# Performance work log

Measured on AMD Instinct MI355X. Metric: run time of the kernel, lower is better.

## Reference

```python
import jax, jax.numpy as jnp
import numpy as np

B, P, E, H = 16, 1024, 1024, 16
DH = E // H  # 64


def setup_inputs() -> dict:
    key = jax.random.key(0)
    ks = jax.random.split(key, 7)
    # kaiming_uniform on [H, DH, DH]: bound = sqrt(6 / fan_in), fan_in = DH
    bound = float(np.sqrt(6.0 / DH))
    w_att_val = jax.random.uniform(ks[0], (H, DH, DH), jnp.float32, -bound, bound)
    attention_bias = jax.random.normal(ks[1], (H, P, P), jnp.float32)
    lb = float(1.0 / np.sqrt(E))
    wv_w = jax.random.uniform(ks[2], (E, E), jnp.float32, -lb, lb)
    wv_b = jax.random.uniform(ks[3], (E,), jnp.float32, -lb, lb)
    out_w = jax.random.uniform(ks[4], (E, E), jnp.float32, -lb, lb)
    out_b = jax.random.uniform(ks[5], (E,), jnp.float32, -lb, lb)
    x = jax.random.normal(ks[6], (B, P, E), jnp.float32)
    return {"x": x, "w_att_val": w_att_val, "attention_bias": attention_bias,
            "wv_w": wv_w, "wv_b": wv_b, "out_w": out_w, "out_b": out_b}


def reference(x, w_att_val, attention_bias, wv_w, wv_b, out_w, out_b):
    b, p, e = x.shape
    dh = e // H
    # split heads: [B, H, P, DH]
    x_h = x.reshape(b, p, H, dh).transpose(0, 2, 1, 3)
    # bilinear scores: (x_h @ W) @ x_h^T -> [B, H, P, P]
    xw = jnp.einsum('bhpd,hde->bhpe', x_h, w_att_val)
    scores = jnp.einsum('bhpe,bhqe->bhpq', xw, x_h)
    scores = scores / jnp.sqrt(jnp.asarray(dh, x.dtype)) + attention_bias
    attn = jax.nn.softmax(scores, axis=-1)
    # values: Linear(E, E) then split heads
    vx = x @ wv_w.T + wv_b
    vx = vx.reshape(b, p, H, dh).transpose(0, 2, 1, 3)
    out = jnp.einsum('bhpq,bhqd->bhpd', attn, vx)
    out = out.transpose(0, 2, 1, 3).reshape(b, p, e)
    return out @ out_w.T + out_b
```

## Files before the change

kernel.cpp:

```cpp
#include <hip/hip_runtime.h>

#define PB 16
#define PP 1024
#define PE 1024
#define PH 16
#define PDH 64

typedef __attribute__((ext_vector_type(8))) short bf16x8;
typedef __attribute__((ext_vector_type(4))) short bf16x4;
typedef __attribute__((ext_vector_type(4))) float f32x4;

#define LOG2E 1.44269504088896340736f

__device__ __forceinline__ short f2bf(float f) {
    union { float f; unsigned u; } a;
    a.f = f;
    unsigned u = a.u;
    u += 0x7fffu + ((u >> 16) & 1u);
    return (short)(u >> 16);
}
__device__ __forceinline__ float bf2f(short s) {
    union { unsigned u; float f; } a;
    a.u = ((unsigned)(unsigned short)s) << 16;
    return a.f;
}
__device__ __forceinline__ unsigned cvtpk(float lo, float hi) {
    unsigned r;
    asm("v_cvt_pk_bf16_f32 %0, %1, %2" : "=v"(r) : "v"(lo), "v"(hi));
    return r;
}
union U8 { unsigned u[4]; bf16x8 v; };
__device__ __forceinline__ void async16(const void* g, void* l) {
    __builtin_amdgcn_global_load_lds(
        (const __attribute__((address_space(1))) unsigned int*)g,
        (__attribute__((address_space(3))) unsigned int*)l, 16, 0, 0);
}

__global__ __launch_bounds__(256) void bias_prep(const float* __restrict__ bias,
                                                 short* __restrict__ biasP) {
    int bid = blockIdx.x;
    int h = bid >> 7, qblk = (bid >> 4) & 7, tile = bid & 15;
    int q0 = qblk * 128, kv0 = tile * 64;
    __shared__ short T[128][68];

    int t = threadIdx.x;
    {
        int qr = t >> 1, half = t & 1;
        const float* src = bias + ((size_t)h << 20) + (size_t)(q0 + qr) * 1024 + kv0 + half * 32;
#pragma unroll
        for (int i = 0; i < 32; i += 4) {
            float4 v = *(const float4*)(src + i);
            bf16x4 p = {f2bf(v.x * LOG2E), f2bf(v.y * LOG2E), f2bf(v.z * LOG2E), f2bf(v.w * LOG2E)};
            *(bf16x4*)&T[qr][half * 32 + i] = p;
        }
    }
    __syncthreads();

    int w = t >> 6, l = t & 63, lm = l & 15, lq = l >> 4;
    short* dst = biasP + (((size_t)(h * 16 + tile) * 8 + qblk) * 4 + w) * 2048 + l * 8;
#pragma unroll
    for (int j = 0; j < 4; j++) {
        bf16x4 a = *(const bf16x4*)&T[w * 32 + lm][j * 16 + lq * 4];
        bf16x4 b = *(const bf16x4*)&T[w * 32 + 16 + lm][j * 16 + lq * 4];
        bf16x8 o = {a[0], a[1], a[2], a[3], b[0], b[1], b[2], b[3]};
        *(bf16x8*)(dst + j * 512) = o;
    }
}

__global__ __launch_bounds__(256) void wconv(const float* __restrict__ wvw,
                                             const float* __restrict__ outw,
                                             short* __restrict__ wvwb,
                                             short* __restrict__ outwb) {
    int bid = blockIdx.x;
    const float* src = (bid < 512) ? wvw : outw;
    short* dst = (bid < 512) ? wvwb : outwb;
    int lb = (bid < 512) ? bid : bid - 512;
    size_t idx = ((size_t)lb * 256 + threadIdx.x) * 8;
    float4 a = *(const float4*)(src + idx);
    float4 b = *(const float4*)(src + idx + 4);
    bf16x8 t = {f2bf(a.x), f2bf(a.y), f2bf(a.z), f2bf(a.w),
                f2bf(b.x), f2bf(b.y), f2bf(b.z), f2bf(b.w)};
    *(bf16x8*)(dst + idx) = t;
}

__global__ __launch_bounds__(256) void xw_kernel(const float* __restrict__ x,
                                                 const float* __restrict__ watt,
                                                 short* __restrict__ xw,
                                                 short* __restrict__ xbf) {
    int bid = blockIdx.x;
    int q4 = bid & 3;
    int bh = bid >> 2;
    int h = bh & 15;
    __shared__ short Wt[64][88];

    int tid = threadIdx.x;
    {
        const float* W = watt + (size_t)h * 4096;
        int idx = tid * 16;
        int d = idx >> 6, e0 = idx & 63;
#pragma unroll
        for (int i = 0; i < 16; i += 4) {
            float4 v = *(const float4*)(W + d * 64 + e0 + i);
            Wt[e0 + i + 0][d] = f2bf(v.x);
            Wt[e0 + i + 1][d] = f2bf(v.y);
            Wt[e0 + i + 2][d] = f2bf(v.z);
            Wt[e0 + i + 3][d] = f2bf(v.w);
        }
    }
    __syncthreads();

    int wave = tid >> 6, lane = tid & 63;
    int lm = lane & 15, lq = lane >> 4;

    bf16x8 bfr[4][2];
#pragma unroll
    for (int nt = 0; nt < 4; nt++)
#pragma unroll
        for (int kf = 0; kf < 2; kf++)
            bfr[nt][kf] = *(const bf16x8*)&Wt[nt * 16 + lm][kf * 32 + lq * 8];

    int b = bh >> 4;
    const float QSCALE = 0.125f * LOG2E;
    for (int pass = 0; pass < 4; pass++) {
        int p0 = q4 * 256 + pass * 64 + wave * 16;
        const float* xrow = x + ((size_t)(b * 1024 + p0 + lm)) * 1024 + h * 64;
        short* xorow = xbf + ((size_t)(b * 1024 + p0 + lm)) * 1024 + h * 64;
        bf16x8 af[2];
#pragma unroll
        for (int kf = 0; kf < 2; kf++) {
            float4 v0 = *(const float4*)(xrow + kf * 32 + lq * 8);
            float4 v1 = *(const float4*)(xrow + kf * 32 + lq * 8 + 4);
            bf16x8 t;
            t[0] = f2bf(v0.x); t[1] = f2bf(v0.y); t[2] = f2bf(v0.z); t[3] = f2bf(v0.w);
            t[4] = f2bf(v1.x); t[5] = f2bf(v1.y); t[6] = f2bf(v1.z); t[7] = f2bf(v1.w);
            af[kf] = t;
            *(bf16x8*)(xorow + kf * 32 + lq * 8) = t;
        }
#pragma unroll
        for (int nt = 0; nt < 4; nt++) {
            f32x4 acc = {0.f, 0.f, 0.f, 0.f};
            acc = __builtin_amdgcn_mfma_f32_16x16x32_bf16(af[0], bfr[nt][0], acc, 0, 0, 0);
            acc = __builtin_amdgcn_mfma_f32_16x16x32_bf16(af[1], bfr[nt][1], acc, 0, 0, 0);
            size_t base = ((size_t)bh * 1024 + p0 + lq * 4) * 64 + nt * 16 + lm;
#pragma unroll
            for (int r = 0; r < 4; r++)
                xw[base + (size_t)r * 64] = f2bf(acc[r] * QSCALE);
        }
    }
}

__global__ __launch_bounds__(256) void vx_gemm(const short* __restrict__ xbf,
                                               const short* __restrict__ wvwb,
                                               const float* __restrict__ wvb,
                                               short* __restrict__ vt) {
    int logical = (blockIdx.x & 7) * 128 + (blockIdx.x >> 3);
    int mblk = logical >> 3, nblk = logical & 7;
    int m0 = mblk * 128, n0 = nblk * 128;
    __shared__ short As[128 * 32];
    __shared__ short Bs[128 * 32];

    int tid = threadIdx.x;
    int wv = tid >> 6, ln = tid & 63;
    int c0 = wv * 2;
    int rrow = ln >> 2, rseg = (ln & 3) * 8;
    const short* gA = xbf + (size_t)(m0 + c0 * 16 + rrow) * 1024 + rseg;
    const short* gB = wvwb + (size_t)(n0 + c0 * 16 + rrow) * 1024 + rseg;
    short* lA = As + c0 * 512;
    short* lB = Bs + c0 * 512;

    int lane = ln, lm = lane & 15, lq = lane >> 4;
    int wm = (wv >> 1) * 64, wn = (wv & 1) * 64;

    f32x4 acc[4][4];
#pragma unroll
    for (int i = 0; i < 4; i++)
#pragma unroll
        for (int j = 0; j < 4; j++) acc[i][j] = (f32x4){0.f, 0.f, 0.f, 0.f};

    for (int k0 = 0; k0 < 1024; k0 += 32) {
        __syncthreads();
        async16(gA + k0, lA);
        async16(gA + k0 + 16 * 1024, lA + 512);
        async16(gB + k0, lB);
        async16(gB + k0 + 16 * 1024, lB + 512);
        __syncthreads();
        bf16x8 af[4], bfr[4];
#pragma unroll
        for (int mt = 0; mt < 4; mt++) af[mt] = *(const bf16x8*)&As[(wm + mt * 16 + lm) * 32 + lq * 8];
#pragma unroll
        for (int nt = 0; nt < 4; nt++) bfr[nt] = *(const bf16x8*)&Bs[(wn + nt * 16 + lm) * 32 + lq * 8];
#pragma unroll
        for (int mt = 0; mt < 4; mt++)
#pragma unroll
            for (int nt = 0; nt < 4; nt++)
                acc[mt][nt] = __builtin_amdgcn_mfma_f32_16x16x32_bf16(af[mt], bfr[nt], acc[mt][nt], 0, 0, 0);
    }

#pragma unroll
    for (int nt = 0; nt < 4; nt++) {
        int e = n0 + wn + nt * 16 + lm;
        float bias = wvb[e];
        int hh = e >> 6, dd = e & 63;
#pragma unroll
        for (int mt = 0; mt < 4; mt++) {
            int pg = m0 + wm + mt * 16 + lq * 4;
            int bb = pg >> 10, pp = pg & 1023;
            bf16x4 pk;
#pragma unroll
            for (int r = 0; r < 4; r++) pk[r] = f2bf(acc[mt][nt][r] + bias);
            *(bf16x4*)(vt + ((size_t)((bb * 16 + hh) * 64 + dd)) * 1024 + pp) = pk;
        }
    }
}

__global__ __launch_bounds__(256, 3) void flash_kernel(const short* __restrict__ xbf,
                                                       const short* __restrict__ xw,
                                                       const short* __restrict__ vt,
                                                       const short* __restrict__ biasP,
                                                       short* __restrict__ obuf) {
    int logical = (blockIdx.x & 7) * 256 + (blockIdx.x >> 3);
    int qblk = logical & 7, b = (logical >> 3) & 15, h = logical >> 7;
    int bh = b * 16 + h;
    int q0 = qblk * 128;

    __shared__ short Ks[64][72];
    __shared__ short Vs[64][72];
    __shared__ float Rs[4][36];

    int tid = threadIdx.x, wave = tid >> 6, lane = tid & 63;
    int lm = lane & 15, lq = lane >> 4;

    bf16x8 qa[2][2];
#pragma unroll
    for (int qt = 0; qt < 2; qt++)
#pragma unroll
        for (int kf = 0; kf < 2; kf++)
            qa[qt][kf] = *(const bf16x8*)(xw + ((size_t)bh * 1024 + q0 + wave * 32 + qt * 16 + lm) * 64 + kf * 32 + lq * 8);

    f32x4 o[2][4];
#pragma unroll
    for (int qt = 0; qt < 2; qt++)
#pragma unroll
        for (int dt = 0; dt < 4; dt++) o[qt][dt] = (f32x4){0.f, 0.f, 0.f, 0.f};
    float rs[2] = {0.f, 0.f};

    int ci0 = tid * 2, ci1 = tid * 2 + 1;
    int r0 = ci0 >> 3, s0 = (ci0 & 7) * 8;
    int r1 = ci1 >> 3, s1 = (ci1 & 7) * 8;
    const short* kg = xbf + ((size_t)(b * 1024)) * 1024 + h * 64;
    const short* vg = vt + ((size_t)bh * 64) * 1024;
    const short* bg = biasP + (((size_t)(h * 16) * 8 + qblk) * 4 + wave) * 2048 + lane * 8;
    const size_t BT_STRIDE = 65536;

    bf16x8 kr[2], vr[2];
    bf16x8 br[4];
    kr[0] = *(const bf16x8*)(kg + (size_t)r0 * 1024 + s0);
    kr[1] = *(const bf16x8*)(kg + (size_t)r1 * 1024 + s1);
    vr[0] = *(const bf16x8*)(vg + (size_t)r0 * 1024 + s0);
    vr[1] = *(const bf16x8*)(vg + (size_t)r1 * 1024 + s1);
#pragma unroll
    for (int kt = 0; kt < 4; kt++)
        br[kt] = *(const bf16x8*)(bg + kt * 512);
    *(bf16x8*)&Ks[r0][s0] = kr[0];
    *(bf16x8*)&Ks[r1][s1] = kr[1];
    *(bf16x8*)&Vs[r0][s0] = vr[0];
    *(bf16x8*)&Vs[r1][s1] = vr[1];

    for (int tile = 0; tile < 16; tile++) {
        int kv0 = tile * 64;
        __syncthreads();

        f32x4 s[4][2];
#pragma unroll
        for (int kt = 0; kt < 4; kt++)
#pragma unroll
            for (int qt = 0; qt < 2; qt++) {
                s[kt][qt] = (f32x4){bf2f(br[kt][qt * 4 + 0]), bf2f(br[kt][qt * 4 + 1]),
                                    bf2f(br[kt][qt * 4 + 2]), bf2f(br[kt][qt * 4 + 3])};
            }

        if (tile < 15) {
            int kvn = kv0 + 64;
            kr[0] = *(const bf16x8*)(kg + (size_t)(kvn + r0) * 1024 + s0);
            kr[1] = *(const bf16x8*)(kg + (size_t)(kvn + r1) * 1024 + s1);
            vr[0] = *(const bf16x8*)(vg + (size_t)r0 * 1024 + kvn + s0);
            vr[1] = *(const bf16x8*)(vg + (size_t)r1 * 1024 + kvn + s1);
            const short* bgn = bg + (size_t)(tile + 1) * BT_STRIDE;
#pragma unroll
            for (int kt = 0; kt < 4; kt++)
                br[kt] = *(const bf16x8*)(bgn + kt * 512);
        }

#pragma unroll
        for (int kf = 0; kf < 2; kf++) {
            bf16x8 ka[4];
#pragma unroll
            for (int kt = 0; kt < 4; kt++)
                ka[kt] = *(const bf16x8*)&Ks[kt * 16 + lm][kf * 32 + lq * 8];
#pragma unroll
            for (int kt = 0; kt < 4; kt++)
#pragma unroll
                for (int qt = 0; qt < 2; qt++)
                    s[kt][qt] = __builtin_amdgcn_mfma_f32_16x16x32_bf16(ka[kt], qa[qt][kf], s[kt][qt], 0, 0, 0);
        }

#pragma unroll
        for (int kt = 0; kt < 4; kt++)
#pragma unroll
            for (int qt = 0; qt < 2; qt++)
#pragma unroll
                for (int r = 0; r < 4; r++) {
                    float pv = __builtin_amdgcn_exp2f(s[kt][qt][r]);
                    s[kt][qt][r] = pv;
                    rs[qt] += pv;
                }

#pragma unroll
        for (int kf = 0; kf < 2; kf++) {
            bf16x8 pa[2];
#pragma unroll
            for (int qt = 0; qt < 2; qt++) {
                U8 u;
                u.u[0] = cvtpk(s[kf * 2][qt][0], s[kf * 2][qt][1]);
                u.u[1] = cvtpk(s[kf * 2][qt][2], s[kf * 2][qt][3]);
                u.u[2] = cvtpk(s[kf * 2 + 1][qt][0], s[kf * 2 + 1][qt][1]);
                u.u[3] = cvtpk(s[kf * 2 + 1][qt][2], s[kf * 2 + 1][qt][3]);
                pa[qt] = u.v;
            }
#pragma unroll
            for (int dt = 0; dt < 4; dt++) {
                U8 uv;
                *(bf16x4*)&uv.u[0] = *(const bf16x4*)&Vs[dt * 16 + lm][kf * 32 + lq * 4];
                *(bf16x4*)&uv.u[2] = *(const bf16x4*)&Vs[dt * 16 + lm][kf * 32 + 16 + lq * 4];
#pragma unroll
                for (int qt = 0; qt < 2; qt++)
                    o[qt][dt] = __builtin_amdgcn_mfma_f32_16x16x32_bf16(pa[qt], uv.v, o[qt][dt], 0, 0, 0);
            }
        }

        __syncthreads();
        if (tile < 15) {
            *(bf16x8*)&Ks[r0][s0] = kr[0];
            *(bf16x8*)&Ks[r1][s1] = kr[1];
            *(bf16x8*)&Vs[r0][s0] = vr[0];
            *(bf16x8*)&Vs[r1][s1] = vr[1];
        }
    }

#pragma unroll
    for (int qt = 0; qt < 2; qt++) {
        rs[qt] += __shfl_xor(rs[qt], 16);
        rs[qt] += __shfl_xor(rs[qt], 32);
    }
    if (lq == 0) { Rs[wave][lm] = rs[0]; Rs[wave][16 + lm] = rs[1]; }
    __syncthreads();

#pragma unroll
    for (int qt = 0; qt < 2; qt++) {
        float inv[4];
#pragma unroll
        for (int r = 0; r < 4; r++)
            inv[r] = 1.f / Rs[wave][qt * 16 + lq * 4 + r];
#pragma unroll
        for (int dt = 0; dt < 4; dt++) {
            int e = h * 64 + dt * 16 + lm;
#pragma unroll
            for (int r = 0; r < 4; r++) {
                int p = q0 + wave * 32 + qt * 16 + lq * 4 + r;
                obuf[((size_t)(b * 1024 + p)) * 1024 + e] = f2bf(o[qt][dt][r] * inv[r]);
            }
        }
    }
}

__global__ __launch_bounds__(256) void out_gemm(const short* __restrict__ obuf,
                                                const short* __restrict__ outwb,
                                                const float* __restrict__ outb,
                                                float* __restrict__ out) {
    int logical = (blockIdx.x & 7) * 128 + (blockIdx.x >> 3);
    int mblk = logical >> 3, nblk = logical & 7;
    int m0 = mblk * 128, n0 = nblk * 128;
    __shared__ short As[128 * 32];
    __shared__ short Bs[128 * 32];

    int tid = threadIdx.x;
    int wv = tid >> 6, ln = tid & 63;
    int c0 = wv * 2;
    int rrow = ln >> 2, rseg = (ln & 3) * 8;
    const short* gA = obuf + (size_t)(m0 + c0 * 16 + rrow) * 1024 + rseg;
    const short* gB = outwb + (size_t)(n0 + c0 * 16 + rrow) * 1024 + rseg;
    short* lA = As + c0 * 512;
    short* lB = Bs + c0 * 512;

    int lm = ln & 15, lq = ln >> 4;
    int wm = (wv >> 1) * 64, wn = (wv & 1) * 64;

    f32x4 acc[4][4];
#pragma unroll
    for (int i = 0; i < 4; i++)
#pragma unroll
        for (int j = 0; j < 4; j++) acc[i][j] = (f32x4){0.f, 0.f, 0.f, 0.f};

    for (int k0 = 0; k0 < 1024; k0 += 32) {
        __syncthreads();
        async16(gA + k0, lA);
        async16(gA + k0 + 16 * 1024, lA + 512);
        async16(gB + k0, lB);
        async16(gB + k0 + 16 * 1024, lB + 512);
        __syncthreads();
        bf16x8 af[4], bfr[4];
#pragma unroll
        for (int mt = 0; mt < 4; mt++) af[mt] = *(const bf16x8*)&As[(wm + mt * 16 + lm) * 32 + lq * 8];
#pragma unroll
        for (int nt = 0; nt < 4; nt++) bfr[nt] = *(const bf16x8*)&Bs[(wn + nt * 16 + lm) * 32 + lq * 8];
#pragma unroll
        for (int mt = 0; mt < 4; mt++)
#pragma unroll
            for (int nt = 0; nt < 4; nt++)
                acc[mt][nt] = __builtin_amdgcn_mfma_f32_16x16x32_bf16(af[mt], bfr[nt], acc[mt][nt], 0, 0, 0);
    }

#pragma unroll
    for (int nt = 0; nt < 4; nt++) {
        int e = n0 + wn + nt * 16 + lm;
        float bias = outb[e];
#pragma unroll
        for (int mt = 0; mt < 4; mt++) {
            int pg = m0 + wm + mt * 16 + lq * 4;
#pragma unroll
            for (int r = 0; r < 4; r++)
                out[(size_t)(pg + r) * 1024 + e] = acc[mt][nt][r] + bias;
        }
    }
}

extern "C" void kernel_launch(void* const* d_in, const int* in_sizes, int n_in,
                              void* d_out, int out_size, void* d_ws, size_t ws_size,
                              hipStream_t stream) {
    const float* x    = (const float*)d_in[0];
    const float* watt = (const float*)d_in[1];
    const float* bias = (const float*)d_in[2];
    const float* wvw  = (const float*)d_in[3];
    const float* wvb  = (const float*)d_in[4];
    const float* outw = (const float*)d_in[5];
    const float* outb = (const float*)d_in[6];
    float* out = (float*)d_out;

    char* ws = (char*)d_ws;
    short* xw     = (short*)ws;
    short* vt     = (short*)(ws + ((size_t)32 << 20));
    short* obuf   = (short*)(ws + ((size_t)64 << 20));
    short* xbf    = (short*)(ws + ((size_t)96 << 20));
    short* biasP  = (short*)(ws + ((size_t)128 << 20));
    short* wvwb   = (short*)(ws + ((size_t)160 << 20));
    short* outwb  = (short*)(ws + ((size_t)162 << 20));

    xw_kernel<<<PB * PH * 4, 256, 0, stream>>>(x, watt, xw, xbf);
    bias_prep<<<2048, 256, 0, stream>>>(bias, biasP);
    wconv<<<1024, 256, 0, stream>>>(wvw, outw, wvwb, outwb);
    vx_gemm<<<(PB * PP / 128) * (PE / 128), 256, 0, stream>>>(xbf, wvwb, wvb, vt);
    flash_kernel<<<PB * PH * (PP / 128), 256, 0, stream>>>(xbf, xw, vt, biasP, obuf);
    out_gemm<<<(PB * PP / 128) * (PE / 128), 256, 0, stream>>>(obuf, outwb, outb, out);
}
```

Baseline: 379.3 us.

## Double-buffer K/V tiles in flash kernel and permute V layout for 16-byte reads

Switches the flash kernel's K/V shared-memory staging to two buffers. The next tile is written before compute and loads run two tiles ahead, so each iteration needs one barrier instead of two. The value projection's store order is permuted within 32-position groups so each lane can read its V fragment with a single 16-byte LDS load instead of two 8-byte loads. The exp row-sum is also split into two partial accumulators to shorten the dependency chain. The cost is doubled LDS for K/V, which may lower occupancy, and more registers held live for the prefetch.

```diff
diff --git a/kernel.cpp b/kernel.cpp
--- a/kernel.cpp
+++ b/kernel.cpp
@@ -30,6 +30,9 @@
     return r;
 }
 union U8 { unsigned u[4]; bf16x8 v; };
+__device__ __forceinline__ void barrier_lds() {
+    asm volatile("s_waitcnt lgkmcnt(0)\n\ts_barrier" ::: "memory");
+}
 __device__ __forceinline__ void async16(const void* g, void* l) {
     __builtin_amdgcn_global_load_lds(
         (const __attribute__((address_space(1))) unsigned int*)g,
@@ -204,7 +207,8 @@
 #pragma unroll
         for (int mt = 0; mt < 4; mt++) {
             int pg = m0 + wm + mt * 16 + lq * 4;
-            int bb = pg >> 10, pp = pg & 1023;
+            int ppn = (pg & ~31) + lq * 8 + (mt & 1) * 4;
+            int bb = ppn >> 10, pp = ppn & 1023;
             bf16x4 pk;
 #pragma unroll
             for (int r = 0; r < 4; r++) pk[r] = f2bf(acc[mt][nt][r] + bias);
@@ -223,8 +227,8 @@
     int bh = b * 16 + h;
     int q0 = qblk * 128;
 
-    __shared__ short Ks[64][72];
-    __shared__ short Vs[64][72];
+    __shared__ short Ks[2][64 * 72];
+    __shared__ short Vs[2][64 * 72];
     __shared__ float Rs[4][36];
 
     int tid = threadIdx.x, wave = tid >> 6, lane = tid & 63;
@@ -242,7 +246,7 @@
     for (int qt = 0; qt < 2; qt++)
 #pragma unroll
         for (int dt = 0; dt < 4; dt++) o[qt][dt] = (f32x4){0.f, 0.f, 0.f, 0.f};
-    float rs[2] = {0.f, 0.f};
+    float2 rs2[2] = {{0.f, 0.f}, {0.f, 0.f}};
 
     int ci0 = tid * 2, ci1 = tid * 2 + 1;
     int r0 = ci0 >> 3, s0 = (ci0 & 7) * 8;
@@ -252,39 +256,68 @@
     const short* bg = biasP + (((size_t)(h * 16) * 8 + qblk) * 4 + wave) * 2048 + lane * 8;
     const size_t BT_STRIDE = 65536;
 
-    bf16x8 kr[2], vr[2];
-    bf16x8 br[4];
+    bf16x8 kr[2], vr[2], br[4];
     kr[0] = *(const bf16x8*)(kg + (size_t)r0 * 1024 + s0);
     kr[1] = *(const bf16x8*)(kg + (size_t)r1 * 1024 + s1);
     vr[0] = *(const bf16x8*)(vg + (size_t)r0 * 1024 + s0);
     vr[1] = *(const bf16x8*)(vg + (size_t)r1 * 1024 + s1);
+    *(bf16x8*)&Ks[0][r0 * 72 + s0] = kr[0];
+    *(bf16x8*)&Ks[0][r1 * 72 + s1] = kr[1];
+    *(bf16x8*)&Vs[0][r0 * 72 + s0] = vr[0];
+    *(bf16x8*)&Vs[0][r1 * 72 + s1] = vr[1];
+    kr[0] = *(const bf16x8*)(kg + (size_t)(64 + r0) * 1024 + s0);
+    kr[1] = *(const bf16x8*)(kg + (size_t)(64 + r1) * 1024 + s1);
+    vr[0] = *(const bf16x8*)(vg + (size_t)r0 * 1024 + 64 + s0);
+    vr[1] = *(const bf16x8*)(vg + (size_t)r1 * 1024 + 64 + s1);
 #pragma unroll
     for (int kt = 0; kt < 4; kt++)
         br[kt] = *(const bf16x8*)(bg + kt * 512);
-    *(bf16x8*)&Ks[r0][s0] = kr[0];
-    *(bf16x8*)&Ks[r1][s1] = kr[1];
-    *(bf16x8*)&Vs[r0][s0] = vr[0];
-    *(bf16x8*)&Vs[r1][s1] = vr[1];
 
     for (int tile = 0; tile < 16; tile++) {
-        int kv0 = tile * 64;
-        __syncthreads();
-
-        f32x4 s[4][2];
-#pragma unroll
-        for (int kt = 0; kt < 4; kt++)
-#pragma unroll
-            for (int qt = 0; qt < 2; qt++) {
-                s[kt][qt] = (f32x4){bf2f(br[kt][qt * 4 + 0]), bf2f(br[kt][qt * 4 + 1]),
-                                    bf2f(br[kt][qt * 4 + 2]), bf2f(br[kt][qt * 4 + 3])};
-            }
+        const int cur = tile & 1;
+        const short* Kc = Ks[cur];
+        const short* Vc = Vs[cur];
+        short* Kn = Ks[cur ^ 1];
+        short* Vn = Vs[cur ^ 1];
+
+        barrier_lds();
 
         if (tile < 15) {
-            int kvn = kv0 + 64;
+            *(bf16x8*)&Kn[r0 * 72 + s0] = kr[0];
+            *(bf16x8*)&Kn[r1 * 72 + s1] = kr[1];
+            *(bf16x8*)&Vn[r0 * 72 + s0] = vr[0];
+            *(bf16x8*)&Vn[r1 * 72 + s1] = vr[1];
+        }
+        if (tile < 14) {
+            int kvn = (tile + 2) * 64;
             kr[0] = *(const bf16x8*)(kg + (size_t)(kvn + r0) * 1024 + s0);
             kr[1] = *(const bf16x8*)(kg + (size_t)(kvn + r1) * 1024 + s1);
             vr[0] = *(const bf16x8*)(vg + (size_t)r0 * 1024 + kvn + s0);
             vr[1] = *(const bf16x8*)(vg + (size_t)r1 * 1024 + kvn + s1);
+        }
+
+        f32x4 s[4][2];
+#pragma unroll
+        for (int kt = 0; kt < 4; kt++)
+#pragma unroll
+            for (int qt = 0; qt < 2; qt++)
+                s[kt][qt] = (f32x4){bf2f(br[kt][qt * 4 + 0]), bf2f(br[kt][qt * 4 + 1]),
+                                    bf2f(br[kt][qt * 4 + 2]), bf2f(br[kt][qt * 4 + 3])};
+
+#pragma unroll
+        for (int kf = 0; kf < 2; kf++) {
+            bf16x8 ka[4];
+#pragma unroll
+            for (int kt = 0; kt < 4; kt++)
+                ka[kt] = *(const bf16x8*)&Kc[(kt * 16 + lm) * 72 + kf * 32 + lq * 8];
+#pragma unroll
+            for (int kt = 0; kt < 4; kt++)
+#pragma unroll
+                for (int qt = 0; qt < 2; qt++)
+                    s[kt][qt] = __builtin_amdgcn_mfma_f32_16x16x32_bf16(ka[kt], qa[qt][kf], s[kt][qt], 0, 0, 0);
+        }
+
+        if (tile < 15) {
             const short* bgn = bg + (size_t)(tile + 1) * BT_STRIDE;
 #pragma unroll
             for (int kt = 0; kt < 4; kt++)
@@ -292,28 +325,17 @@
         }
 
 #pragma unroll
-        for (int kf = 0; kf < 2; kf++) {
-            bf16x8 ka[4];
-#pragma unroll
-            for (int kt = 0; kt < 4; kt++)
-                ka[kt] = *(const bf16x8*)&Ks[kt * 16 + lm][kf * 32 + lq * 8];
-#pragma unroll
-            for (int kt = 0; kt < 4; kt++)
-#pragma unroll
-                for (int qt = 0; qt < 2; qt++)
-                    s[kt][qt] = __builtin_amdgcn_mfma_f32_16x16x32_bf16(ka[kt], qa[qt][kf], s[kt][qt], 0, 0, 0);
-        }
-
-#pragma unroll
         for (int kt = 0; kt < 4; kt++)
 #pragma unroll
-            for (int qt = 0; qt < 2; qt++)
-#pragma unroll
-                for (int r = 0; r < 4; r++) {
-                    float pv = __builtin_amdgcn_exp2f(s[kt][qt][r]);
-                    s[kt][qt][r] = pv;
-                    rs[qt] += pv;
-                }
+            for (int qt = 0; qt < 2; qt++) {
+                float p0 = __builtin_amdgcn_exp2f(s[kt][qt][0]);
+                float p1 = __builtin_amdgcn_exp2f(s[kt][qt][1]);
+                float p2 = __builtin_amdgcn_exp2f(s[kt][qt][2]);
+                float p3 = __builtin_amdgcn_exp2f(s[kt][qt][3]);
+                s[kt][qt] = (f32x4){p0, p1, p2, p3};
+                rs2[qt].x += p0 + p2;
+                rs2[qt].y += p1 + p3;
+            }
 
 #pragma unroll
         for (int kf = 0; kf < 2; kf++) {
@@ -329,24 +351,15 @@
             }
 #pragma unroll
             for (int dt = 0; dt < 4; dt++) {
-                U8 uv;
-                *(bf16x4*)&uv.u[0] = *(const bf16x4*)&Vs[dt * 16 + lm][kf * 32 + lq * 4];
-                *(bf16x4*)&uv.u[2] = *(const bf16x4*)&Vs[dt * 16 + lm][kf * 32 + 16 + lq * 4];
+                bf16x8 uv = *(const bf16x8*)&Vc[(dt * 16 + lm) * 72 + kf * 32 + lq * 8];
 #pragma unroll
                 for (int qt = 0; qt < 2; qt++)
-                    o[qt][dt] = __builtin_amdgcn_mfma_f32_16x16x32_bf16(pa[qt], uv.v, o[qt][dt], 0, 0, 0);
+                    o[qt][dt] = __builtin_amdgcn_mfma_f32_16x16x32_bf16(pa[qt], uv, o[qt][dt], 0, 0, 0);
             }
         }
-
-        __syncthreads();
-        if (tile < 15) {
-            *(bf16x8*)&Ks[r0][s0] = kr[0];
-            *(bf16x8*)&Ks[r1][s1] = kr[1];
-            *(bf16x8*)&Vs[r0][s0] = vr[0];
-            *(bf16x8*)&Vs[r1][s1] = vr[1];
-        }
-    }
-
+    }
+
+    float rs[2] = {rs2[0].x + rs2[0].y, rs2[1].x + rs2[1].y};
 #pragma unroll
     for (int qt = 0; qt < 2; qt++) {
         rs[qt] += __shfl_xor(rs[qt], 16);
```

New measurement: 380.9 us. Within noise of the previous version (+0.4%).
